# Kernel optimization log

Hardware: AMD Instinct MI355X
Metric: run time of the kernel (lower is better)

Reference implementation:

```python
import jax, jax.numpy as jnp
import numpy as np
from jax import lax
from jax.scipy.special import ndtri
from jax.scipy.stats import norm

# Hyperparameters from __init__ defaults (num_inputs=8)
MU_A = 0.99          # sigmoid(logit_mu_a)
SIGMA_A = 0.1
A_MAX = 1.0          # truncation upper bound (module-level constant in repo)
SIGMASQ0 = 1.0       # initial-state variance (module-level constant in repo)
SIGMA_MU_X = 1.0
MU_W = 0.0
SIGMA_W = 1.0

S, T, D = 512, 8192, 8


def setup_inputs() -> dict:
    key = jax.random.key(0)
    ks = jax.random.split(key, 8)
    return dict(
        inputs=jax.random.normal(ks[0], (S, T, D), jnp.float32),
        eps_w=jax.random.normal(ks[1], (S, D), jnp.float32),
        u_a=jax.random.uniform(ks[2], (S,), jnp.float32, 1e-4, 1.0 - 1e-4),
        sigmasq=jax.random.uniform(ks[3], (S,), jnp.float32, 0.01, 0.3),
        eps_mu=jax.random.normal(ks[4], (S,), jnp.float32),
        eps_x0=jax.random.normal(ks[5], (S,), jnp.float32),
        eps_x=jax.random.normal(ks[6], (S, T), jnp.float32),
        u_bern=jax.random.uniform(ks[7], (S, T), jnp.float32),
    )


def reference(inputs, eps_w, u_a, sigmasq, eps_mu, eps_x0, eps_x, u_bern):
    # Per-subject parameter draws (reparameterized)
    w = MU_W + SIGMA_W * eps_w                              # [S, D]  Normal(mu_w, sigma_w)
    # TruncatedNormal(MU_A, SIGMA_A, 0, A_MAX) via inverse CDF
    alpha = (0.0 - MU_A) / SIGMA_A
    beta = (A_MAX - MU_A) / SIGMA_A
    Fa, Fb = norm.cdf(alpha), norm.cdf(beta)
    a = MU_A + SIGMA_A * ndtri(Fa + u_a * (Fb - Fa))        # [S]
    mu_x = SIGMA_MU_X * eps_mu                              # [S]  Normal(0, sigma_mu_x)
    b = mu_x * (1.0 - a)                                    # [S]
    x0 = mu_x + jnp.sqrt(SIGMASQ0) * eps_x0                 # [S]
    sd = jnp.sqrt(sigmasq)                                  # [S]

    # AR(1) latent scan over trials, vectorized over subjects.
    # Matches original: outputs collect x_t BEFORE the update, i.e. x_0..x_{T-1}.
    def step(x, eps_t):
        x_next = a * x + b + sd * eps_t
        return x_next, x

    _, xs = lax.scan(step, x0, eps_x.T)                     # xs: [T, S]
    x = xs.T                                                # [S, T]

    logits = x + jnp.einsum('std,sd->st', inputs, w)        # [S, T]
    y = (u_bern < jax.nn.sigmoid(logits)).astype(jnp.int32) # Bernoulli(logits) sample
    return x, y
```

## Files before the change

### kernel.cpp

```cpp
#include <hip/hip_runtime.h>
#include <cmath>

#define S_SUB 512
#define T_TR  8192
#define D_IN  8
#define NSEG  4
#define SEGT  (T_TR/NSEG)
#define BLK   256
#define CH    (SEGT/BLK)
#define NW    (BLK/64)

typedef float f4 __attribute__((ext_vector_type(4)));

__global__ void setup_kernel(const float* __restrict__ u_a,
                             const float* __restrict__ sigmasq,
                             const float* __restrict__ eps_mu,
                             const float* __restrict__ eps_x0,
                             double Fa, double dF,
                             double* __restrict__ params) {
    int s = blockIdx.x * blockDim.x + threadIdx.x;
    if (s >= S_SUB) return;
    const double RS2 = 0.7071067811865476;
    const double S2  = 1.4142135623730951;
    const double ISQ = 0.3989422804014327;
    double p = fma((double)u_a[s], dF, Fa);
    double z = -S2 * erfcinv(2.0 * p);
    #pragma unroll
    for (int it = 0; it < 2; ++it) {
        double F   = 0.5 * erfc(-z * RS2);
        double pdf = exp(-0.5 * z * z) * ISQ;
        z -= (F - p) / pdf;
    }
    double a  = 0.99 + 0.1 * z;
    double mu = (double)eps_mu[s];
    double b  = mu * (1.0 - a);
    double x0 = mu + (double)eps_x0[s];
    double sd = sqrt((double)sigmasq[s]);
    params[4*s+0] = a;
    params[4*s+1] = b;
    params[4*s+2] = sd;
    params[4*s+3] = x0;
}

__global__ __launch_bounds__(BLK, 8) void mono_kernel(
    const float* __restrict__ inputs,
    const float* __restrict__ eps_w,
    const float* __restrict__ eps_x,
    const float* __restrict__ u_bern,
    const double* __restrict__ params,
    float* __restrict__ out_x,
    float* __restrict__ out_y)
{
    const int bid  = blockIdx.x;
    const int s    = bid >> 2;
    const int seg  = bid & 3;
    const int tid  = threadIdx.x;
    const int lane = tid & 63;
    const int wid  = tid >> 6;

    __shared__ double2 wtot[NW];
    __shared__ double  xs[BLK * (CH + 1)];

    const size_t subjbase = (size_t)s * T_TR;
    const size_t segbase  = subjbase + (size_t)seg * SEGT;
    const size_t base     = segbase + (size_t)tid * CH;

    const f4* e4 = (const f4*)(eps_x + base);
    f4 o0 = e4[0];
    f4 o1 = e4[1];
    f4 q0[3], q1[3];
    #pragma unroll
    for (int p = 0; p < NSEG - 1; ++p) {
        if (p < seg) {
            const f4* ep = (const f4*)(eps_x + subjbase + (size_t)p * SEGT
                                       + (size_t)tid * CH);
            q0[p] = ep[0];
            q1[p] = ep[1];
        }
    }

    const double a  = params[4*s+0];
    const double b  = params[4*s+1];
    const double sd = params[4*s+2];
    double xseed    = params[4*s+3];

    #pragma unroll
    for (int p = 0; p < NSEG - 1; ++p) {
        if (p < seg) {
            float evp[CH];
            evp[0]=q0[p].x; evp[1]=q0[p].y; evp[2]=q0[p].z; evp[3]=q0[p].w;
            evp[4]=q1[p].x; evp[5]=q1[p].y; evp[6]=q1[p].z; evp[7]=q1[p].w;
            double A = 1.0, Bv = 0.0;
            #pragma unroll
            for (int j = 0; j < CH; ++j) {
                double c = fma(sd, (double)evp[j], b);
                Bv = fma(a, Bv, c);
                A *= a;
            }
            #pragma unroll
            for (int off = 1; off < 64; off <<= 1) {
                double pA = __shfl_down(A, off);
                double pB = __shfl_down(Bv, off);
                Bv = fma(pA, Bv, pB);
                A  = pA * A;
            }
            if (lane == 0) wtot[wid] = make_double2(A, Bv);
            __syncthreads();
            double CA = wtot[0].x, CB = wtot[0].y;
            #pragma unroll
            for (int w = 1; w < NW; ++w) {
                CB = fma(wtot[w].x, CB, wtot[w].y);
                CA = wtot[w].x * CA;
            }
            xseed = fma(CA, xseed, CB);
            __syncthreads();
        }
    }

    float ev[CH];
    ev[0]=o0.x; ev[1]=o0.y; ev[2]=o0.z; ev[3]=o0.w;
    ev[4]=o1.x; ev[5]=o1.y; ev[6]=o1.z; ev[7]=o1.w;

    double A = 1.0, Bv = 0.0;
    #pragma unroll
    for (int j = 0; j < CH; ++j) {
        double c = fma(sd, (double)ev[j], b);
        Bv = fma(a, Bv, c);
        A *= a;
    }
    #pragma unroll
    for (int off = 1; off < 64; off <<= 1) {
        double pA = __shfl_up(A, off);
        double pB = __shfl_up(Bv, off);
        if (lane >= off) {
            Bv = fma(A, pB, Bv);
            A  = A * pA;
        }
    }
    if (lane == 63) wtot[wid] = make_double2(A, Bv);
    __syncthreads();

    double PA = 1.0, PB = 0.0;
    for (int w = 0; w < wid; ++w) {
        double2 t = wtot[w];
        PB = fma(t.x, PB, t.y);
        PA = t.x * PA;
    }
    double eA = __shfl_up(A, 1);
    double eB = __shfl_up(Bv, 1);
    if (lane == 0) { eA = 1.0; eB = 0.0; }
    double EB = fma(eA, PB, eB);
    double EA = eA * PA;
    double x  = fma(EA, xseed, EB);

    #pragma unroll
    for (int j = 0; j < CH; ++j) {
        xs[tid * (CH + 1) + j] = x;
        double c = fma(sd, (double)ev[j], b);
        x = fma(a, x, c);
    }
    __syncthreads();

    const float* wp = eps_w + s * D_IN;
    const double w0 = (double)wp[0], w1 = (double)wp[1];
    const double w2 = (double)wp[2], w3 = (double)wp[3];
    const double w4 = (double)wp[4], w5 = (double)wp[5];
    const double w6 = (double)wp[6], w7 = (double)wp[7];

    float uv[CH];
    #pragma unroll
    for (int j = 0; j < CH; ++j)
        uv[j] = u_bern[segbase + j * BLK + tid];

    const f4* in4 = (const f4*)(inputs + segbase * D_IN);
    #pragma unroll
    for (int j = 0; j < CH; ++j) {
        const int t = j * BLK + tid;
        f4 i0 = in4[2*t];
        f4 i1 = in4[2*t + 1];
        double xv = xs[(t >> 3) * (CH + 1) + (t & 7)];
        double dot = fma((double)i0.x, w0,
                     fma((double)i0.y, w1,
                     fma((double)i0.z, w2,
                     fma((double)i0.w, w3,
                     fma((double)i1.x, w4,
                     fma((double)i1.y, w5,
                     fma((double)i1.z, w6, (double)i1.w * w7)))))));
        double L = xv + dot;
        double E = exp(-L);
        out_y[segbase + t] = ((double)uv[j] * (1.0 + E) < 1.0) ? 1.0f : 0.0f;
        out_x[segbase + t] = (float)xv;
    }
}

extern "C" void kernel_launch(void* const* d_in, const int* in_sizes, int n_in,
                              void* d_out, int out_size, void* d_ws, size_t ws_size,
                              hipStream_t stream) {
    const float* inputs  = (const float*)d_in[0];
    const float* eps_w   = (const float*)d_in[1];
    const float* u_a     = (const float*)d_in[2];
    const float* sigmasq = (const float*)d_in[3];
    const float* eps_mu  = (const float*)d_in[4];
    const float* eps_x0  = (const float*)d_in[5];
    const float* eps_x   = (const float*)d_in[6];
    const float* u_bern  = (const float*)d_in[7];

    float*  out    = (float*)d_out;
    double* params = (double*)d_ws;

    const double RS2 = 0.7071067811865476;
    const double Fa  = 0.5 * erfc(9.9 * RS2);
    const double Fb  = 0.5 * erfc(-0.1 * RS2);
    const double dF  = Fb - Fa;

    setup_kernel<<<2, 256, 0, stream>>>(u_a, sigmasq, eps_mu, eps_x0, Fa, dF, params);
    mono_kernel<<<S_SUB*NSEG, BLK, 0, stream>>>(inputs, eps_w, eps_x, u_bern,
                                                params,
                                                out, out + (size_t)S_SUB * T_TR);
}
```

Baseline: 43.93 us.

## Replace redundant prefix-segment recomputation with cooperative grid sync exchange

Before, each segment block recomputed the affine composition of all preceding segments by itself. Now each block publishes its own segment's composed (A,B) to global memory, a cooperative grid sync follows, and the block then chains the earlier segments' results to get its seed. If the cooperative launch fails, a two-kernel fallback (compose, then fused) is used. Phase B is also changed to vectorized float4 loads of u_bern and float4 stores of x and y, with each thread handling contiguous timesteps. The grid sync needs all 2048 blocks to be resident at once, and it adds global barrier latency.

```diff
diff --git a/kernel.cpp b/kernel.cpp
--- a/kernel.cpp
+++ b/kernel.cpp
@@ -1,5 +1,8 @@
 #include <hip/hip_runtime.h>
+#include <hip/hip_cooperative_groups.h>
 #include <cmath>
+
+namespace cg = cooperative_groups;
 
 #define S_SUB 512
 #define T_TR  8192
@@ -42,12 +45,60 @@
     params[4*s+3] = x0;
 }
 
-__global__ __launch_bounds__(BLK, 8) void mono_kernel(
+__device__ __forceinline__ void phaseB(
+    const float* __restrict__ inputs,
+    const float* __restrict__ eps_w,
+    const float* __restrict__ u_bern,
+    const double* __restrict__ xs,
+    size_t segbase, int s, int tid,
+    float* __restrict__ out_x,
+    float* __restrict__ out_y)
+{
+    const float* wp = eps_w + s * D_IN;
+    const double w0 = (double)wp[0], w1 = (double)wp[1];
+    const double w2 = (double)wp[2], w3 = (double)wp[3];
+    const double w4 = (double)wp[4], w5 = (double)wp[5];
+    const double w6 = (double)wp[6], w7 = (double)wp[7];
+
+    const f4* in4 = (const f4*)(inputs + segbase * D_IN);
+    #pragma unroll
+    for (int g = 0; g < CH/4; ++g) {
+        const int t0 = g * (BLK * 4) + tid * 4;
+        f4 ub = *(const f4*)(u_bern + segbase + t0);
+        float ubk[4]; ubk[0]=ub.x; ubk[1]=ub.y; ubk[2]=ub.z; ubk[3]=ub.w;
+        float xk[4], yk[4];
+        #pragma unroll
+        for (int k = 0; k < 4; ++k) {
+            const int t = t0 + k;
+            f4 i0 = in4[2*t];
+            f4 i1 = in4[2*t+1];
+            double xv = xs[(t >> 3) * (CH + 1) + (t & 7)];
+            double dot = fma((double)i0.x, w0,
+                         fma((double)i0.y, w1,
+                         fma((double)i0.z, w2,
+                         fma((double)i0.w, w3,
+                         fma((double)i1.x, w4,
+                         fma((double)i1.y, w5,
+                         fma((double)i1.z, w6, (double)i1.w * w7)))))));
+            double L = xv + dot;
+            double E = exp(-L);
+            yk[k] = ((double)ubk[k] * (1.0 + E) < 1.0) ? 1.0f : 0.0f;
+            xk[k] = (float)xv;
+        }
+        f4 vx; vx.x=xk[0]; vx.y=xk[1]; vx.z=xk[2]; vx.w=xk[3];
+        f4 vy; vy.x=yk[0]; vy.y=yk[1]; vy.z=yk[2]; vy.w=yk[3];
+        *(f4*)(out_x + segbase + t0) = vx;
+        *(f4*)(out_y + segbase + t0) = vy;
+    }
+}
+
+__global__ __launch_bounds__(BLK, 8) void coop_kernel(
     const float* __restrict__ inputs,
     const float* __restrict__ eps_w,
     const float* __restrict__ eps_x,
     const float* __restrict__ u_bern,
     const double* __restrict__ params,
+    double2* __restrict__ comp,
     float* __restrict__ out_x,
     float* __restrict__ out_y)
 {
@@ -61,61 +112,16 @@
     __shared__ double2 wtot[NW];
     __shared__ double  xs[BLK * (CH + 1)];
 
-    const size_t subjbase = (size_t)s * T_TR;
-    const size_t segbase  = subjbase + (size_t)seg * SEGT;
-    const size_t base     = segbase + (size_t)tid * CH;
+    const size_t segbase = (size_t)s * T_TR + (size_t)seg * SEGT;
+    const size_t base    = segbase + (size_t)tid * CH;
 
     const f4* e4 = (const f4*)(eps_x + base);
     f4 o0 = e4[0];
     f4 o1 = e4[1];
-    f4 q0[3], q1[3];
-    #pragma unroll
-    for (int p = 0; p < NSEG - 1; ++p) {
-        if (p < seg) {
-            const f4* ep = (const f4*)(eps_x + subjbase + (size_t)p * SEGT
-                                       + (size_t)tid * CH);
-            q0[p] = ep[0];
-            q1[p] = ep[1];
-        }
-    }
 
     const double a  = params[4*s+0];
     const double b  = params[4*s+1];
     const double sd = params[4*s+2];
-    double xseed    = params[4*s+3];
-
-    #pragma unroll
-    for (int p = 0; p < NSEG - 1; ++p) {
-        if (p < seg) {
-            float evp[CH];
-            evp[0]=q0[p].x; evp[1]=q0[p].y; evp[2]=q0[p].z; evp[3]=q0[p].w;
-            evp[4]=q1[p].x; evp[5]=q1[p].y; evp[6]=q1[p].z; evp[7]=q1[p].w;
-            double A = 1.0, Bv = 0.0;
-            #pragma unroll
-            for (int j = 0; j < CH; ++j) {
-                double c = fma(sd, (double)evp[j], b);
-                Bv = fma(a, Bv, c);
-                A *= a;
-            }
-            #pragma unroll
-            for (int off = 1; off < 64; off <<= 1) {
-                double pA = __shfl_down(A, off);
-                double pB = __shfl_down(Bv, off);
-                Bv = fma(pA, Bv, pB);
-                A  = pA * A;
-            }
-            if (lane == 0) wtot[wid] = make_double2(A, Bv);
-            __syncthreads();
-            double CA = wtot[0].x, CB = wtot[0].y;
-            #pragma unroll
-            for (int w = 1; w < NW; ++w) {
-                CB = fma(wtot[w].x, CB, wtot[w].y);
-                CA = wtot[w].x * CA;
-            }
-            xseed = fma(CA, xseed, CB);
-            __syncthreads();
-        }
-    }
 
     float ev[CH];
     ev[0]=o0.x; ev[1]=o0.y; ev[2]=o0.z; ev[3]=o0.w;
@@ -140,6 +146,164 @@
     if (lane == 63) wtot[wid] = make_double2(A, Bv);
     __syncthreads();
 
+    if (tid == 0 && seg < NSEG - 1) {
+        double TA = wtot[0].x, TB = wtot[0].y;
+        #pragma unroll
+        for (int w = 1; w < NW; ++w) {
+            TB = fma(wtot[w].x, TB, wtot[w].y);
+            TA = wtot[w].x * TA;
+        }
+        comp[seg * S_SUB + s] = make_double2(TA, TB);
+    }
+
+    double PA = 1.0, PB = 0.0;
+    for (int w = 0; w < wid; ++w) {
+        double2 t = wtot[w];
+        PB = fma(t.x, PB, t.y);
+        PA = t.x * PA;
+    }
+    double eA = __shfl_up(A, 1);
+    double eB = __shfl_up(Bv, 1);
+    if (lane == 0) { eA = 1.0; eB = 0.0; }
+    double EB = fma(eA, PB, eB);
+    double EA = eA * PA;
+
+    cg::this_grid().sync();
+
+    double xseed = params[4*s+3];
+    #pragma unroll
+    for (int p = 0; p < NSEG - 1; ++p) {
+        if (p < seg) {
+            double2 c = comp[p * S_SUB + s];
+            xseed = fma(c.x, xseed, c.y);
+        }
+    }
+    double x = fma(EA, xseed, EB);
+
+    #pragma unroll
+    for (int j = 0; j < CH; ++j) {
+        xs[tid * (CH + 1) + j] = x;
+        double c = fma(sd, (double)ev[j], b);
+        x = fma(a, x, c);
+    }
+    __syncthreads();
+
+    phaseB(inputs, eps_w, u_bern, xs, segbase, s, tid, out_x, out_y);
+}
+
+__global__ __launch_bounds__(BLK) void compose2_kernel(
+    const float* __restrict__ eps_x,
+    const double* __restrict__ params,
+    double2* __restrict__ comp)
+{
+    const int bid = blockIdx.x;
+    const int s   = bid / 3;
+    const int seg = bid % 3;
+    const int tid  = threadIdx.x;
+    const int lane = tid & 63;
+    const int wid  = tid >> 6;
+
+    __shared__ double2 wtot[NW];
+    const size_t base = (size_t)s * T_TR + (size_t)seg * SEGT + (size_t)tid * CH;
+
+    const f4* e4 = (const f4*)(eps_x + base);
+    f4 v0 = e4[0];
+    f4 v1 = e4[1];
+
+    const double a  = params[4*s+0];
+    const double b  = params[4*s+1];
+    const double sd = params[4*s+2];
+
+    float ev[CH];
+    ev[0]=v0.x; ev[1]=v0.y; ev[2]=v0.z; ev[3]=v0.w;
+    ev[4]=v1.x; ev[5]=v1.y; ev[6]=v1.z; ev[7]=v1.w;
+
+    double A = 1.0, Bv = 0.0;
+    #pragma unroll
+    for (int j = 0; j < CH; ++j) {
+        double c = fma(sd, (double)ev[j], b);
+        Bv = fma(a, Bv, c);
+        A *= a;
+    }
+    #pragma unroll
+    for (int off = 1; off < 64; off <<= 1) {
+        double pA = __shfl_down(A, off);
+        double pB = __shfl_down(Bv, off);
+        Bv = fma(pA, Bv, pB);
+        A  = pA * A;
+    }
+    if (lane == 0) wtot[wid] = make_double2(A, Bv);
+    __syncthreads();
+    if (tid == 0) {
+        double CA = wtot[0].x, CB = wtot[0].y;
+        #pragma unroll
+        for (int w = 1; w < NW; ++w) {
+            CB = fma(wtot[w].x, CB, wtot[w].y);
+            CA = wtot[w].x * CA;
+        }
+        comp[seg * S_SUB + s] = make_double2(CA, CB);
+    }
+}
+
+__global__ __launch_bounds__(BLK, 8) void fused2_kernel(
+    const float* __restrict__ inputs,
+    const float* __restrict__ eps_w,
+    const float* __restrict__ eps_x,
+    const float* __restrict__ u_bern,
+    const double* __restrict__ params,
+    const double2* __restrict__ comp,
+    float* __restrict__ out_x,
+    float* __restrict__ out_y)
+{
+    const int bid  = blockIdx.x;
+    const int s    = bid >> 2;
+    const int seg  = bid & 3;
+    const int tid  = threadIdx.x;
+    const int lane = tid & 63;
+    const int wid  = tid >> 6;
+
+    __shared__ double2 wtot[NW];
+    __shared__ double  xs[BLK * (CH + 1)];
+
+    const size_t segbase = (size_t)s * T_TR + (size_t)seg * SEGT;
+    const size_t base    = segbase + (size_t)tid * CH;
+
+    const f4* e4 = (const f4*)(eps_x + base);
+    f4 o0 = e4[0];
+    f4 o1 = e4[1];
+
+    const double a  = params[4*s+0];
+    const double b  = params[4*s+1];
+    const double sd = params[4*s+2];
+    double xseed    = params[4*s+3];
+    for (int i = 0; i < seg; ++i) {
+        double2 c = comp[i * S_SUB + s];
+        xseed = fma(c.x, xseed, c.y);
+    }
+
+    float ev[CH];
+    ev[0]=o0.x; ev[1]=o0.y; ev[2]=o0.z; ev[3]=o0.w;
+    ev[4]=o1.x; ev[5]=o1.y; ev[6]=o1.z; ev[7]=o1.w;
+
+    double A = 1.0, Bv = 0.0;
+    #pragma unroll
+    for (int j = 0; j < CH; ++j) {
+        double c = fma(sd, (double)ev[j], b);
+        Bv = fma(a, Bv, c);
+        A *= a;
+    }
+    #pragma unroll
+    for (int off = 1; off < 64; off <<= 1) {
+        double pA = __shfl_up(A, off);
+        double pB = __shfl_up(Bv, off);
+        if (lane >= off) {
+            Bv = fma(A, pB, Bv);
+            A  = A * pA;
+        }
+    }
+    if (lane == 63) wtot[wid] = make_double2(A, Bv);
+    __syncthreads();
+
     double PA = 1.0, PB = 0.0;
     for (int w = 0; w < wid; ++w) {
         double2 t = wtot[w];
@@ -161,36 +325,7 @@
     }
     __syncthreads();
 
-    const float* wp = eps_w + s * D_IN;
-    const double w0 = (double)wp[0], w1 = (double)wp[1];
-    const double w2 = (double)wp[2], w3 = (double)wp[3];
-    const double w4 = (double)wp[4], w5 = (double)wp[5];
-    const double w6 = (double)wp[6], w7 = (double)wp[7];
-
-    float uv[CH];
-    #pragma unroll
-    for (int j = 0; j < CH; ++j)
-        uv[j] = u_bern[segbase + j * BLK + tid];
-
-    const f4* in4 = (const f4*)(inputs + segbase * D_IN);
-    #pragma unroll
-    for (int j = 0; j < CH; ++j) {
-        const int t = j * BLK + tid;
-        f4 i0 = in4[2*t];
-        f4 i1 = in4[2*t + 1];
-        double xv = xs[(t >> 3) * (CH + 1) + (t & 7)];
-        double dot = fma((double)i0.x, w0,
-                     fma((double)i0.y, w1,
-                     fma((double)i0.z, w2,
-                     fma((double)i0.w, w3,
-                     fma((double)i1.x, w4,
-                     fma((double)i1.y, w5,
-                     fma((double)i1.z, w6, (double)i1.w * w7)))))));
-        double L = xv + dot;
-        double E = exp(-L);
-        out_y[segbase + t] = ((double)uv[j] * (1.0 + E) < 1.0) ? 1.0f : 0.0f;
-        out_x[segbase + t] = (float)xv;
-    }
+    phaseB(inputs, eps_w, u_bern, xs, segbase, s, tid, out_x, out_y);
 }
 
 extern "C" void kernel_launch(void* const* d_in, const int* in_sizes, int n_in,
@@ -205,8 +340,11 @@
     const float* eps_x   = (const float*)d_in[6];
     const float* u_bern  = (const float*)d_in[7];
 
-    float*  out    = (float*)d_out;
-    double* params = (double*)d_ws;
+    float*   out    = (float*)d_out;
+    float*   out_x  = out;
+    float*   out_y  = out + (size_t)S_SUB * T_TR;
+    double*  params = (double*)d_ws;
+    double2* comp   = (double2*)((char*)d_ws + 16*1024);
 
     const double RS2 = 0.7071067811865476;
     const double Fa  = 0.5 * erfc(9.9 * RS2);
@@ -214,7 +352,15 @@
     const double dF  = Fb - Fa;
 
     setup_kernel<<<2, 256, 0, stream>>>(u_a, sigmasq, eps_mu, eps_x0, Fa, dF, params);
-    mono_kernel<<<S_SUB*NSEG, BLK, 0, stream>>>(inputs, eps_w, eps_x, u_bern,
-                                                params,
-                                                out, out + (size_t)S_SUB * T_TR);
-}
+
+    void* args[] = { (void*)&inputs, (void*)&eps_w, (void*)&eps_x, (void*)&u_bern,
+                     (void*)&params, (void*)&comp, (void*)&out_x, (void*)&out_y };
+    hipError_t err = hipLaunchCooperativeKernel(
+        (const void*)coop_kernel, dim3(S_SUB * NSEG), dim3(BLK), args, 0, stream);
+
+    if (err != hipSuccess) {
+        compose2_kernel<<<S_SUB*(NSEG-1), BLK, 0, stream>>>(eps_x, params, comp);
+        fused2_kernel<<<S_SUB*NSEG, BLK, 0, stream>>>(inputs, eps_w, eps_x, u_bern,
+                                                      params, comp, out_x, out_y);
+    }
+}
```

Result: slower. 142.0 us (+223.2%).

## Process each subject in a single 1024-thread block instead of four segments

Applied to the files above, without the earlier changes.

Each subject's 8192 trials are now handled by one 1024-thread block rather than four 256-thread blocks. This removes the redundant prefix scans over earlier segments and the extra eps_x reloads, along with the associated block-level synchronisations. The cost is fewer, larger blocks: 512 in total, each using about 74KB of LDS. That leaves less room for occupancy and latency hiding in what is largely a bandwidth-bound kernel. The cross-warp combine is also longer, with up to 15 serial steps.

```diff
diff --git a/kernel.cpp b/kernel.cpp
--- a/kernel.cpp
+++ b/kernel.cpp
@@ -4,10 +4,8 @@
 #define S_SUB 512
 #define T_TR  8192
 #define D_IN  8
-#define NSEG  4
-#define SEGT  (T_TR/NSEG)
-#define BLK   256
-#define CH    (SEGT/BLK)
+#define BLK   1024
+#define CH    (T_TR/BLK)
 #define NW    (BLK/64)
 
 typedef float f4 __attribute__((ext_vector_type(4)));
@@ -51,9 +49,7 @@
     float* __restrict__ out_x,
     float* __restrict__ out_y)
 {
-    const int bid  = blockIdx.x;
-    const int s    = bid >> 2;
-    const int seg  = bid & 3;
+    const int s    = blockIdx.x;
     const int tid  = threadIdx.x;
     const int lane = tid & 63;
     const int wid  = tid >> 6;
@@ -62,60 +58,16 @@
     __shared__ double  xs[BLK * (CH + 1)];
 
     const size_t subjbase = (size_t)s * T_TR;
-    const size_t segbase  = subjbase + (size_t)seg * SEGT;
-    const size_t base     = segbase + (size_t)tid * CH;
+    const size_t base     = subjbase + (size_t)tid * CH;
 
     const f4* e4 = (const f4*)(eps_x + base);
     f4 o0 = e4[0];
     f4 o1 = e4[1];
-    f4 q0[3], q1[3];
-    #pragma unroll
-    for (int p = 0; p < NSEG - 1; ++p) {
-        if (p < seg) {
-            const f4* ep = (const f4*)(eps_x + subjbase + (size_t)p * SEGT
-                                       + (size_t)tid * CH);
-            q0[p] = ep[0];
-            q1[p] = ep[1];
-        }
-    }
 
     const double a  = params[4*s+0];
     const double b  = params[4*s+1];
     const double sd = params[4*s+2];
-    double xseed    = params[4*s+3];
-
-    #pragma unroll
-    for (int p = 0; p < NSEG - 1; ++p) {
-        if (p < seg) {
-            float evp[CH];
-            evp[0]=q0[p].x; evp[1]=q0[p].y; evp[2]=q0[p].z; evp[3]=q0[p].w;
-            evp[4]=q1[p].x; evp[5]=q1[p].y; evp[6]=q1[p].z; evp[7]=q1[p].w;
-            double A = 1.0, Bv = 0.0;
-            #pragma unroll
-            for (int j = 0; j < CH; ++j) {
-                double c = fma(sd, (double)evp[j], b);
-                Bv = fma(a, Bv, c);
-                A *= a;
-            }
-            #pragma unroll
-            for (int off = 1; off < 64; off <<= 1) {
-                double pA = __shfl_down(A, off);
-                double pB = __shfl_down(Bv, off);
-                Bv = fma(pA, Bv, pB);
-                A  = pA * A;
-            }
-            if (lane == 0) wtot[wid] = make_double2(A, Bv);
-            __syncthreads();
-            double CA = wtot[0].x, CB = wtot[0].y;
-            #pragma unroll
-            for (int w = 1; w < NW; ++w) {
-                CB = fma(wtot[w].x, CB, wtot[w].y);
-                CA = wtot[w].x * CA;
-            }
-            xseed = fma(CA, xseed, CB);
-            __syncthreads();
-        }
-    }
+    const double x0 = params[4*s+3];
 
     float ev[CH];
     ev[0]=o0.x; ev[1]=o0.y; ev[2]=o0.z; ev[3]=o0.w;
@@ -128,6 +80,7 @@
         Bv = fma(a, Bv, c);
         A *= a;
     }
+
     #pragma unroll
     for (int off = 1; off < 64; off <<= 1) {
         double pA = __shfl_up(A, off);
@@ -151,7 +104,7 @@
     if (lane == 0) { eA = 1.0; eB = 0.0; }
     double EB = fma(eA, PB, eB);
     double EA = eA * PA;
-    double x  = fma(EA, xseed, EB);
+    double x  = fma(EA, x0, EB);
 
     #pragma unroll
     for (int j = 0; j < CH; ++j) {
@@ -170,9 +123,9 @@
     float uv[CH];
     #pragma unroll
     for (int j = 0; j < CH; ++j)
-        uv[j] = u_bern[segbase + j * BLK + tid];
+        uv[j] = u_bern[subjbase + j * BLK + tid];
 
-    const f4* in4 = (const f4*)(inputs + segbase * D_IN);
+    const f4* in4 = (const f4*)(inputs + subjbase * D_IN);
     #pragma unroll
     for (int j = 0; j < CH; ++j) {
         const int t = j * BLK + tid;
@@ -188,8 +141,8 @@
                      fma((double)i1.z, w6, (double)i1.w * w7)))))));
         double L = xv + dot;
         double E = exp(-L);
-        out_y[segbase + t] = ((double)uv[j] * (1.0 + E) < 1.0) ? 1.0f : 0.0f;
-        out_x[segbase + t] = (float)xv;
+        out_y[subjbase + t] = ((double)uv[j] * (1.0 + E) < 1.0) ? 1.0f : 0.0f;
+        out_x[subjbase + t] = (float)xv;
     }
 }
 
@@ -214,7 +167,6 @@
     const double dF  = Fb - Fa;
 
     setup_kernel<<<2, 256, 0, stream>>>(u_a, sigmasq, eps_mu, eps_x0, Fa, dF, params);
-    mono_kernel<<<S_SUB*NSEG, BLK, 0, stream>>>(inputs, eps_w, eps_x, u_bern,
-                                                params,
-                                                out, out + (size_t)S_SUB * T_TR);
+    mono_kernel<<<S_SUB, BLK, 0, stream>>>(inputs, eps_w, eps_x, u_bern, params,
+                                           out, out + (size_t)S_SUB * T_TR);
 }
```

New measurement: 39.29 us. -10.6%, faster.
